# Kernel optimization log

Measured on AMD Instinct MI355X. Metric: run time of the kernel, lower is better.

Reference implementation:

```python
import jax, jax.numpy as jnp
import numpy as np
from jax import lax

# Dimensions (see shape_source)
B, J, I, E, H = 256, 128, 64, 512, 512   # batch, target len, source len, embed, hidden
MAXJW = 128                               # max jump width
WJ = 2 * MAXJW + 1                        # size of jump-width set (257)
ALPHA_P0 = 1.0
EPS = 1e-29


def setup_inputs() -> dict:
    key = jax.random.key(0)
    ks = jax.random.split(key, 10)
    return {
        "y_hidden": jax.random.normal(ks[0], (B, J, E), jnp.float32),
        "y_hidden_null": jax.random.normal(ks[1], (1, 1, E), jnp.float32),
        "W_trans": jax.random.normal(ks[2], (E, H), jnp.float32) * 0.02,
        "b_trans": jnp.zeros((H,), jnp.float32),
        "W_jump": jax.random.normal(ks[3], (H, WJ), jnp.float32) * 0.02,
        "b_jump": jnp.zeros((WJ,), jnp.float32),
        "W_p0": jax.random.normal(ks[4], (H, 1), jnp.float32) * 0.02,
        "b_p0": jnp.zeros((1,), jnp.float32),
        # emission probs p(source_t | target_state_k), kept near 1 to avoid
        # underflow of the unrescaled HMM forward product (as in original).
        "emission": jax.random.uniform(ks[5], (B, 2 * J, I), jnp.float32) * 0.5 + 0.75,
        "source_lengths": jax.random.randint(ks[6], (B,), 1, I + 1, dtype=jnp.int32),
        "target_lengths": jax.random.randint(ks[7], (B,), 1, J + 1, dtype=jnp.int32),
    }


def _build_transition(y_hidden, y_hidden_null, W_trans, b_trans, W_jump, b_jump, W_p0, b_p0):
    # get_transition: Dense(tanh) -> Dense(softmax) jump widths; Dense(sigmoid) p0.
    ts = jnp.tanh(y_hidden @ W_trans + b_trans)           # [B,J,H]
    ts_null = jnp.tanh(y_hidden_null @ W_trans + b_trans) # [1,1,H]
    jump_prob = jax.nn.softmax(ts @ W_jump + b_jump, axis=-1)  # [B,J,WJ]
    p0_scalar = ALPHA_P0 * jax.nn.sigmoid(ts_null @ W_p0 + b_p0)[0, 0, 0]
    p0 = jnp.broadcast_to(p0_scalar, (y_hidden.shape[0], J))  # tile to [B,J]
    # gather jump widths: row i takes jump_prob[:, i, MAXJW + k - i] for k in [0,J)
    idx = MAXJW + jnp.arange(J)[None, :] - jnp.arange(J)[:, None]        # [J,J]
    idxb = jnp.broadcast_to(idx[None], (jump_prob.shape[0], J, J))
    jw = jnp.take_along_axis(jump_prob, idxb, axis=2)                    # [B,J,J]
    jw = jw * (1.0 - p0[:, :, None]) / jnp.sum(jw, axis=2, keepdims=True)
    diag_p0 = p0[:, :, None] * jnp.eye(J, dtype=jw.dtype)                # [B,J,J]
    T_half = jnp.concatenate([jw, diag_p0], axis=2)                      # [B,J,2J]
    return jnp.concatenate([T_half, T_half], axis=1)                     # [B,2J,2J]


def reference(y_hidden, y_hidden_null, W_trans, b_trans, W_jump, b_jump,
              W_p0, b_p0, emission, source_lengths, target_lengths):
    T = _build_transition(y_hidden, y_hidden_null, W_trans, b_trans,
                          W_jump, b_jump, W_p0, b_p0)       # [B,2J,2J]
    e = jnp.transpose(emission, (2, 0, 1))                  # [I,B,2J]
    # tf.scan with no initializer: f_0 = emission at source position 0
    f0 = e[0]

    def step(f, et):
        f_next = jnp.einsum('bj,bjk->bk', f, T) * et        # forward recursion
        return f_next, f_next

    _, fs = lax.scan(step, f0, e[1:])
    fs = jnp.concatenate([f0[None], fs], axis=0)            # [I,B,2J]
    fbt = jnp.transpose(fs, (1, 2, 0))                      # [B,2J,I]
    last_idx = (source_lengths - 1).astype(jnp.int32)[:, None, None]
    last = jnp.take_along_axis(fbt, last_idx, axis=2)[:, :, 0]  # [B,2J]
    m = (jnp.arange(J)[None, :] < target_lengths[:, None]).astype(last.dtype)
    mask = jnp.concatenate([m, m], axis=1)                  # [B,2J]
    return jnp.log(jnp.sum(last * mask, axis=1) + EPS)      # [B]
```

## Files before the change

kernel.cpp:

```cpp
#include <hip/hip_runtime.h>
#include <stdint.h>

typedef __attribute__((ext_vector_type(8))) short bf16x8;
typedef __attribute__((ext_vector_type(4))) float f32x4;

__device__ __forceinline__ unsigned short f2bf(float f) {
  union { float f; unsigned int u; } un; un.f = f;
  unsigned int r = un.u + 0x7fffu + ((un.u >> 16) & 1u);
  return (unsigned short)(r >> 16);
}

__device__ __forceinline__ float tanh_fast(float x) {
  x = fminf(15.f, fmaxf(-15.f, x));
  float e = __expf(2.f * x);
  return (e - 1.f) / (e + 1.f);
}

__device__ __forceinline__ unsigned int cvt_pk_bf16(float lo, float hi) {
  unsigned int r;
  asm("v_cvt_pk_bf16_f32 %0, %1, %2" : "=v"(r) : "v"(lo), "v"(hi));
  return r;
}

__device__ __forceinline__ void gload_lds16(const void* g, void* l) {
  __builtin_amdgcn_global_load_lds(
      (const __attribute__((address_space(1))) unsigned int*)(unsigned long long)g,
      (__attribute__((address_space(3))) unsigned int*)(unsigned int)(unsigned long long)l,
      16, 0, 0);
}

__global__ __launch_bounds__(256) void cvt_transpose_kernel(
    const float* __restrict__ W, unsigned short* __restrict__ Wt,
    int R, int C, int ldW) {
  int i = blockIdx.x * blockDim.x + threadIdx.x;
  if (i < R * C) {
    int c = i / R, r = i - c * R;
    Wt[(size_t)c * R + r] = f2bf(W[(size_t)r * ldW + c]);
  }
}

__global__ __launch_bounds__(512) void p0_kernel(
    const float* __restrict__ ynull, const float* __restrict__ W_trans,
    const float* __restrict__ b_trans, const float* __restrict__ W_p0,
    const float* __restrict__ b_p0, float* __restrict__ p0buf) {
  __shared__ float red[512];
  const int hh = threadIdx.x;
  float acc = 0.f;
  for (int e = 0; e < 512; ++e) acc = fmaf(ynull[e], W_trans[(size_t)e * 512 + hh], acc);
  const float ts = tanhf(acc + b_trans[hh]);
  red[hh] = ts * W_p0[hh];
  __syncthreads();
  for (int s = 256; s > 0; s >>= 1) {
    if (hh < s) red[hh] += red[hh + s];
    __syncthreads();
  }
  if (hh == 0) {
    const float z = red[0] + b_p0[0];
    const float p0 = 1.f / (1.f + __expf(-z));
    p0buf[0] = p0;
    p0buf[1] = 1.f - p0;
  }
}


__global__ __launch_bounds__(256, 2) void gemm_af32(
    const float* __restrict__ A, const unsigned short* __restrict__ Bt,
    const float* __restrict__ bias, unsigned short* __restrict__ Cout,
    int M, int N, int K) {
  __shared__ unsigned short sA[128 * 32];
  __shared__ unsigned short sB[128 * 32];
  const int tid = threadIdx.x;
  const int lane = tid & 63;
  const int wave = tid >> 6;
  const int wr = wave >> 1, wc = wave & 1;
  const int m0 = blockIdx.x * 128, n0 = blockIdx.y * 128;

  f32x4 acc[4][4] = {};

  const int srow = lane >> 2;
  const int sl = lane & 3;
  const int scol = sl * 8;
  const int wsz = (srow >> 1) & 3;
  const int scolw = (sl ^ wsz) * 8;
  const int c0 = wave * 2, c1 = wave * 2 + 1;
  const float* Af0 = A + (size_t)(m0 + c0 * 16 + srow) * K + scol;
  const float* Af1 = A + (size_t)(m0 + c1 * 16 + srow) * K + scol;
  const unsigned short* Br0 = Bt + (size_t)(n0 + c0 * 16 + srow) * K + scolw;
  const unsigned short* Br1 = Bt + (size_t)(n0 + c1 * 16 + srow) * K + scolw;

  float4 a00 = *reinterpret_cast<const float4*>(Af0);
  float4 a01 = *reinterpret_cast<const float4*>(Af0 + 4);
  float4 a10 = *reinterpret_cast<const float4*>(Af1);
  float4 a11 = *reinterpret_cast<const float4*>(Af1 + 4);

  const int r15 = lane & 15;
  const int oslot = (((lane >> 4) ^ ((r15 >> 1) & 3))) * 8;

  for (int kk = 0; kk < K; kk += 32) {
    __syncthreads();
    {
      union { unsigned int u[4]; bf16x8 v; } p;
      p.u[0] = cvt_pk_bf16(a00.x, a00.y);
      p.u[1] = cvt_pk_bf16(a00.z, a00.w);
      p.u[2] = cvt_pk_bf16(a01.x, a01.y);
      p.u[3] = cvt_pk_bf16(a01.z, a01.w);
      *reinterpret_cast<bf16x8*>(&sA[c0 * 512 + srow * 32 + scolw]) = p.v;
      p.u[0] = cvt_pk_bf16(a10.x, a10.y);
      p.u[1] = cvt_pk_bf16(a10.z, a10.w);
      p.u[2] = cvt_pk_bf16(a11.x, a11.y);
      p.u[3] = cvt_pk_bf16(a11.z, a11.w);
      *reinterpret_cast<bf16x8*>(&sA[c1 * 512 + srow * 32 + scolw]) = p.v;
    }
    gload_lds16(Br0 + kk, &sB[c0 * 512]);
    gload_lds16(Br1 + kk, &sB[c1 * 512]);
    __syncthreads();
    if (kk + 32 < K) {
      a00 = *reinterpret_cast<const float4*>(Af0 + kk + 32);
      a01 = *reinterpret_cast<const float4*>(Af0 + kk + 36);
      a10 = *reinterpret_cast<const float4*>(Af1 + kk + 32);
      a11 = *reinterpret_cast<const float4*>(Af1 + kk + 36);
    }
    bf16x8 af[4], bfr[4];
#pragma unroll
    for (int mi = 0; mi < 4; ++mi)
      af[mi] = *reinterpret_cast<const bf16x8*>(
          &sA[(wr * 64 + mi * 16 + r15) * 32 + oslot]);
#pragma unroll
    for (int ni = 0; ni < 4; ++ni)
      bfr[ni] = *reinterpret_cast<const bf16x8*>(
          &sB[(wc * 64 + ni * 16 + r15) * 32 + oslot]);
#pragma unroll
    for (int mi = 0; mi < 4; ++mi)
#pragma unroll
      for (int ni = 0; ni < 4; ++ni)
        acc[mi][ni] = __builtin_amdgcn_mfma_f32_16x16x32_bf16(
            af[mi], bfr[ni], acc[mi][ni], 0, 0, 0);
  }

  const int crow0 = m0 + wr * 64 + (lane >> 4) * 4;
  const int ccol0 = n0 + wc * 64 + r15;
#pragma unroll
  for (int mi = 0; mi < 4; ++mi) {
#pragma unroll
    for (int ni = 0; ni < 4; ++ni) {
      const int gcol = ccol0 + ni * 16;
      const float bv = bias[gcol];
#pragma unroll
      for (int r = 0; r < 4; ++r) {
        const int grow = crow0 + mi * 16 + r;
        Cout[(size_t)grow * N + gcol] = f2bf(tanh_fast(acc[mi][ni][r] + bv));
      }
    }
  }
}

__global__ __launch_bounds__(256, 2) void gemm_tt(
    const unsigned short* __restrict__ A, const unsigned short* __restrict__ Bt,
    const float* __restrict__ bias, float* __restrict__ Cout,
    int M, int N, int K) {
  __shared__ unsigned short sA[128 * 32];
  __shared__ unsigned short sB[128 * 32];
  const int tid = threadIdx.x;
  const int lane = tid & 63;
  const int wave = tid >> 6;
  const int wr = wave >> 1, wc = wave & 1;
  const int m0 = blockIdx.x * 128, n0 = blockIdx.y * 128;

  f32x4 acc[4][4] = {};

  const int srow = lane >> 2;
  const int sl = lane & 3;
  const int wsz = (srow >> 1) & 3;
  const int scolw = (sl ^ wsz) * 8;
  const int c0 = wave * 2, c1 = wave * 2 + 1;
  const unsigned short* Ar0 = A + (size_t)(m0 + c0 * 16 + srow) * K + scolw;
  const unsigned short* Ar1 = A + (size_t)(m0 + c1 * 16 + srow) * K + scolw;
  const unsigned short* Br0 = Bt + (size_t)(n0 + c0 * 16 + srow) * K + scolw;
  const unsigned short* Br1 = Bt + (size_t)(n0 + c1 * 16 + srow) * K + scolw;

  const int r15 = lane & 15;
  const int oslot = (((lane >> 4) ^ ((r15 >> 1) & 3))) * 8;

  for (int kk = 0; kk < K; kk += 32) {
    __syncthreads();
    gload_lds16(Ar0 + kk, &sA[c0 * 512]);
    gload_lds16(Ar1 + kk, &sA[c1 * 512]);
    gload_lds16(Br0 + kk, &sB[c0 * 512]);
    gload_lds16(Br1 + kk, &sB[c1 * 512]);
    __syncthreads();
    bf16x8 af[4], bfr[4];
#pragma unroll
    for (int mi = 0; mi < 4; ++mi)
      af[mi] = *reinterpret_cast<const bf16x8*>(
          &sA[(wr * 64 + mi * 16 + r15) * 32 + oslot]);
#pragma unroll
    for (int ni = 0; ni < 4; ++ni)
      bfr[ni] = *reinterpret_cast<const bf16x8*>(
          &sB[(wc * 64 + ni * 16 + r15) * 32 + oslot]);
#pragma unroll
    for (int mi = 0; mi < 4; ++mi)
#pragma unroll
      for (int ni = 0; ni < 4; ++ni)
        acc[mi][ni] = __builtin_amdgcn_mfma_f32_16x16x32_bf16(
            af[mi], bfr[ni], acc[mi][ni], 0, 0, 0);
  }

  const int crow0 = m0 + wr * 64 + (lane >> 4) * 4;
  const int ccol0 = n0 + wc * 64 + r15;
#pragma unroll
  for (int mi = 0; mi < 4; ++mi) {
#pragma unroll
    for (int ni = 0; ni < 4; ++ni) {
      const int gcol = ccol0 + ni * 16;
      const float bv = bias[gcol];
#pragma unroll
      for (int r = 0; r < 4; ++r) {
        const int grow = crow0 + mi * 16 + r;
        Cout[(size_t)grow * N + gcol] = acc[mi][ni][r] + bv;
      }
    }
  }
}

__global__ __launch_bounds__(256) void wsoftmax_kernel(
    const float* __restrict__ logits, const float* __restrict__ p0buf,
    unsigned short* __restrict__ jwout) {
  const int lane = threadIdx.x & 63;
  const int wave = threadIdx.x >> 6;
  const int row = blockIdx.x * 4 + wave;
  const int i = row & 127;
  const float* lrow = logits + (size_t)row * 256 + (128 - i);
  const float v0 = lrow[lane];
  const float v1 = lrow[lane + 64];
  float mx = fmaxf(v0, v1);
#pragma unroll
  for (int off = 32; off > 0; off >>= 1) mx = fmaxf(mx, __shfl_xor(mx, off));
  const float e0 = __expf(v0 - mx);
  const float e1 = __expf(v1 - mx);
  float s = e0 + e1;
#pragma unroll
  for (int off = 32; off > 0; off >>= 1) s += __shfl_xor(s, off);
  const float scale = p0buf[1] / s;
  unsigned short* orow = jwout + (size_t)row * 128;
  orow[lane] = f2bf(e0 * scale);
  orow[lane + 64] = f2bf(e1 * scale);
}

#define SE_STRIDE 264
__global__ __launch_bounds__(256, 1) void forward_fused(
    const unsigned short* __restrict__ jwb,
    const float* __restrict__ emission,
    const float* __restrict__ p0buf, const int* __restrict__ slen_p,
    const int* __restrict__ tlen_p, float* __restrict__ out) {
  __shared__ __align__(16) float se[64 * SE_STRIDE];
  __shared__ __align__(16) unsigned short gl16[128];
  const int b = blockIdx.x;
  const int tid = threadIdx.x;
  const float* eb = emission + (size_t)b * 16384;

  bf16x8 bfr[4][8];
  const int l = tid & 63;
  const int m = l & 15;
  const int q = l >> 4;

  if (tid >= 64) {
#pragma unroll
    for (int it = 0; it < 6; ++it) {
      const int tau = (tid - 64) + 192 * it;
      if (tau < 1024) {
        const int t0 = (tau & 15) * 4;
        const int mm = (tau >> 4) & 15;
        const int nt0 = ((tau >> 8) & 1) * 4;
        const int half = (tau >> 9) & 1;
        const int kbase = half * 128 + nt0 * 16 + mm;
        const float4 v0 = *reinterpret_cast<const float4*>(&eb[(size_t)(kbase) * 64 + t0]);
        const float4 v1 = *reinterpret_cast<const float4*>(&eb[(size_t)(kbase + 16) * 64 + t0]);
        const float4 v2 = *reinterpret_cast<const float4*>(&eb[(size_t)(kbase + 32) * 64 + t0]);
        const float4 v3 = *reinterpret_cast<const float4*>(&eb[(size_t)(kbase + 48) * 64 + t0]);
        const int jinv0 = half * 128 + mm * 8 + nt0;
        float* d = &se[(size_t)t0 * SE_STRIDE + jinv0];
        *reinterpret_cast<float4*>(d) = (float4){v0.x, v1.x, v2.x, v3.x};
        *reinterpret_cast<float4*>(d + SE_STRIDE) = (float4){v0.y, v1.y, v2.y, v3.y};
        *reinterpret_cast<float4*>(d + 2 * SE_STRIDE) = (float4){v0.z, v1.z, v2.z, v3.z};
        *reinterpret_cast<float4*>(d + 3 * SE_STRIDE) = (float4){v0.w, v1.w, v2.w, v3.w};
      }
    }
  } else {
    const unsigned short* jwt = jwb + (size_t)b * 16384;
#pragma unroll
    for (int kt = 0; kt < 4; ++kt) {
      const int r0 = kt * 32 + q * 8;
#pragma unroll
      for (int nt = 0; nt < 8; ++nt) {
        const int c = nt * 16 + m;
        bf16x8 v;
#pragma unroll
        for (int j = 0; j < 8; ++j) v[j] = (short)jwt[(size_t)(r0 + j) * 128 + c];
        bfr[kt][nt] = v;
      }
    }
  }
  __syncthreads();
  if (tid >= 64) return;

  const float p0 = p0buf[0];
  const int S = slen_p[b];
  const int T = tlen_p[b];

  float gown[8];
  {
    const float4 i0a = *reinterpret_cast<const float4*>(&se[m * 8]);
    const float4 i0b = *reinterpret_cast<const float4*>(&se[m * 8 + 4]);
    const float4 i1a = *reinterpret_cast<const float4*>(&se[128 + m * 8]);
    const float4 i1b = *reinterpret_cast<const float4*>(&se[128 + m * 8 + 4]);
    gown[0] = i0a.x + i1a.x; gown[1] = i0a.y + i1a.y;
    gown[2] = i0a.z + i1a.z; gown[3] = i0a.w + i1a.w;
    gown[4] = i0b.x + i1b.x; gown[5] = i0b.y + i1b.y;
    gown[6] = i0b.z + i1b.z; gown[7] = i0b.w + i1b.w;
  }
  gl16[(2 * q) * 16 + m]     = f2bf(gown[2 * q]);
  gl16[(2 * q + 1) * 16 + m] = f2bf(gown[2 * q + 1]);

  for (int t = 1; t < S; ++t) {
    const float* st = &se[(size_t)t * SE_STRIDE];
    const float4 pe0a = *reinterpret_cast<const float4*>(&st[m * 8]);
    const float4 pe0b = *reinterpret_cast<const float4*>(&st[m * 8 + 4]);
    const float4 pe1a = *reinterpret_cast<const float4*>(&st[128 + m * 8]);
    const float4 pe1b = *reinterpret_cast<const float4*>(&st[128 + m * 8 + 4]);
    const float e0[8] = {pe0a.x, pe0a.y, pe0a.z, pe0a.w, pe0b.x, pe0b.y, pe0b.z, pe0b.w};
    const float e1[8] = {pe1a.x, pe1a.y, pe1a.z, pe1a.w, pe1b.x, pe1b.y, pe1b.z, pe1b.w};
    float h[8];
#pragma unroll
    for (int nt = 0; nt < 8; ++nt) h[nt] = gown[nt] * (p0 * e1[nt]);
    bf16x8 af[4];
#pragma unroll
    for (int kt = 0; kt < 4; ++kt)
      af[kt] = *reinterpret_cast<const bf16x8*>(&gl16[kt * 32 + q * 8]);
    f32x4 acc[8];
#pragma unroll
    for (int nt = 0; nt < 8; ++nt) {
      f32x4 a = __builtin_amdgcn_mfma_f32_16x16x32_bf16(
          af[0], bfr[0][nt], (f32x4){0.f, 0.f, 0.f, 0.f}, 0, 0, 0);
      a = __builtin_amdgcn_mfma_f32_16x16x32_bf16(af[1], bfr[1][nt], a, 0, 0, 0);
      a = __builtin_amdgcn_mfma_f32_16x16x32_bf16(af[2], bfr[2][nt], a, 0, 0, 0);
      acc[nt] = __builtin_amdgcn_mfma_f32_16x16x32_bf16(af[3], bfr[3][nt], a, 0, 0, 0);
    }
#pragma unroll
    for (int nt = 0; nt < 8; ++nt) gown[nt] = fmaf(acc[nt][0], e0[nt], h[nt]);
    gl16[(2 * q) * 16 + m]     = f2bf(gown[2 * q]);
    gl16[(2 * q + 1) * 16 + m] = f2bf(gown[2 * q + 1]);
  }

  float val = 0.f;
#pragma unroll
  for (int nt = 0; nt < 8; ++nt)
    if (nt * 16 + m < T) val += gown[nt];
#pragma unroll
  for (int off = 1; off < 16; off <<= 1) val += __shfl_xor(val, off);
  if (l == 0) out[b] = logf(val + 1e-29f);
}

extern "C" void kernel_launch(void* const* d_in, const int* in_sizes, int n_in,
                              void* d_out, int out_size, void* d_ws, size_t ws_size,
                              hipStream_t stream) {
  const float* y_hidden = (const float*)d_in[0];
  const float* y_null   = (const float*)d_in[1];
  const float* W_trans  = (const float*)d_in[2];
  const float* b_trans  = (const float*)d_in[3];
  const float* W_jump   = (const float*)d_in[4];
  const float* b_jump   = (const float*)d_in[5];
  const float* W_p0     = (const float*)d_in[6];
  const float* b_p0     = (const float*)d_in[7];
  const float* emission = (const float*)d_in[8];
  const int* slen = (const int*)d_in[9];
  const int* tlen = (const int*)d_in[10];
  float* out = (float*)d_out;

  char* ws = (char*)d_ws;
  float* logits         = (float*)ws;
  unsigned short* ts16  = (unsigned short*)(ws + 33554432);
  unsigned short* wt16t = (unsigned short*)(ws + 67108864);
  unsigned short* wj16t = (unsigned short*)(ws + 67633152);
  float* p0buf          = (float*)(ws + 67895296);
  unsigned short* jwb16 = (unsigned short*)(ws + 67895552);

  cvt_transpose_kernel<<<dim3((512 * 512 + 255) / 256), dim3(256), 0, stream>>>(
      W_trans, wt16t, 512, 512, 512);
  cvt_transpose_kernel<<<dim3((512 * 256 + 255) / 256), dim3(256), 0, stream>>>(
      W_jump, wj16t, 512, 256, 257);
  p0_kernel<<<dim3(1), dim3(512), 0, stream>>>(y_null, W_trans, b_trans, W_p0, b_p0, p0buf);

  gemm_af32<<<dim3(256, 4), dim3(256), 0, stream>>>(y_hidden, wt16t, b_trans, ts16,
                                                    32768, 512, 512);
  gemm_tt<<<dim3(256, 2), dim3(256), 0, stream>>>(ts16, wj16t, b_jump, logits,
                                                  32768, 256, 512);
  wsoftmax_kernel<<<dim3(8192), dim3(256), 0, stream>>>(logits, p0buf, jwb16);
  forward_fused<<<dim3(256), dim3(256), 0, stream>>>(jwb16, emission, p0buf,
                                                     slen, tlen, out);
}
```

Measured before the change: 118.6 us.

## Double-buffer GEMM LDS staging, store logits as bf16, merge weight conversion kernels

Result: faster. 116.2 us (-2.0%).

```diff
diff --git a/kernel.cpp b/kernel.cpp
--- a/kernel.cpp
+++ b/kernel.cpp
@@ -8,6 +8,11 @@
   union { float f; unsigned int u; } un; un.f = f;
   unsigned int r = un.u + 0x7fffu + ((un.u >> 16) & 1u);
   return (unsigned short)(r >> 16);
+}
+
+__device__ __forceinline__ float bf2f(unsigned short u) {
+  union { unsigned int u; float f; } un; un.u = ((unsigned int)u) << 16;
+  return un.f;
 }
 
 __device__ __forceinline__ float tanh_fast(float x) {
@@ -29,13 +34,17 @@
       16, 0, 0);
 }
 
-__global__ __launch_bounds__(256) void cvt_transpose_kernel(
-    const float* __restrict__ W, unsigned short* __restrict__ Wt,
-    int R, int C, int ldW) {
-  int i = blockIdx.x * blockDim.x + threadIdx.x;
-  if (i < R * C) {
-    int c = i / R, r = i - c * R;
-    Wt[(size_t)c * R + r] = f2bf(W[(size_t)r * ldW + c]);
+__global__ __launch_bounds__(256) void cvt_weights(
+    const float* __restrict__ Wt_in, const float* __restrict__ Wj_in,
+    unsigned short* __restrict__ wt, unsigned short* __restrict__ wj) {
+  const int i = blockIdx.x * 256 + threadIdx.x;
+  if (i < 512 * 512) {
+    const int c = i >> 9, r = i & 511;
+    wt[i] = f2bf(Wt_in[(size_t)r * 512 + c]);
+  } else {
+    const int j = i - 512 * 512;
+    const int c = j >> 9, r = j & 511;
+    wj[j] = f2bf(Wj_in[(size_t)r * 257 + c]);
   }
 }
 
@@ -67,8 +76,8 @@
     const float* __restrict__ A, const unsigned short* __restrict__ Bt,
     const float* __restrict__ bias, unsigned short* __restrict__ Cout,
     int M, int N, int K) {
-  __shared__ unsigned short sA[128 * 32];
-  __shared__ unsigned short sB[128 * 32];
+  __shared__ unsigned short sA[2][128 * 32];
+  __shared__ unsigned short sB[2][128 * 32];
   const int tid = threadIdx.x;
   const int lane = tid & 63;
   const int wave = tid >> 6;
@@ -88,53 +97,83 @@
   const unsigned short* Br0 = Bt + (size_t)(n0 + c0 * 16 + srow) * K + scolw;
   const unsigned short* Br1 = Bt + (size_t)(n0 + c1 * 16 + srow) * K + scolw;
 
-  float4 a00 = *reinterpret_cast<const float4*>(Af0);
-  float4 a01 = *reinterpret_cast<const float4*>(Af0 + 4);
-  float4 a10 = *reinterpret_cast<const float4*>(Af1);
-  float4 a11 = *reinterpret_cast<const float4*>(Af1 + 4);
-
   const int r15 = lane & 15;
-  const int oslot = (((lane >> 4) ^ ((r15 >> 1) & 3))) * 8;
-
-  for (int kk = 0; kk < K; kk += 32) {
-    __syncthreads();
-    {
-      union { unsigned int u[4]; bf16x8 v; } p;
-      p.u[0] = cvt_pk_bf16(a00.x, a00.y);
-      p.u[1] = cvt_pk_bf16(a00.z, a00.w);
-      p.u[2] = cvt_pk_bf16(a01.x, a01.y);
-      p.u[3] = cvt_pk_bf16(a01.z, a01.w);
-      *reinterpret_cast<bf16x8*>(&sA[c0 * 512 + srow * 32 + scolw]) = p.v;
-      p.u[0] = cvt_pk_bf16(a10.x, a10.y);
-      p.u[1] = cvt_pk_bf16(a10.z, a10.w);
-      p.u[2] = cvt_pk_bf16(a11.x, a11.y);
-      p.u[3] = cvt_pk_bf16(a11.z, a11.w);
-      *reinterpret_cast<bf16x8*>(&sA[c1 * 512 + srow * 32 + scolw]) = p.v;
-    }
-    gload_lds16(Br0 + kk, &sB[c0 * 512]);
-    gload_lds16(Br1 + kk, &sB[c1 * 512]);
-    __syncthreads();
-    if (kk + 32 < K) {
-      a00 = *reinterpret_cast<const float4*>(Af0 + kk + 32);
-      a01 = *reinterpret_cast<const float4*>(Af0 + kk + 36);
-      a10 = *reinterpret_cast<const float4*>(Af1 + kk + 32);
-      a11 = *reinterpret_cast<const float4*>(Af1 + kk + 36);
-    }
+  const int oslot = ((lane >> 4) ^ ((r15 >> 1) & 3)) * 8;
+  const int nt = K >> 5;
+
+  auto writeA = [&](int bi, const float4& v00, const float4& v01,
+                    const float4& v10, const float4& v11) {
+    union { unsigned int u[4]; bf16x8 v; } p;
+    p.u[0] = cvt_pk_bf16(v00.x, v00.y);
+    p.u[1] = cvt_pk_bf16(v00.z, v00.w);
+    p.u[2] = cvt_pk_bf16(v01.x, v01.y);
+    p.u[3] = cvt_pk_bf16(v01.z, v01.w);
+    *reinterpret_cast<bf16x8*>(&sA[bi][c0 * 512 + srow * 32 + scolw]) = p.v;
+    p.u[0] = cvt_pk_bf16(v10.x, v10.y);
+    p.u[1] = cvt_pk_bf16(v10.z, v10.w);
+    p.u[2] = cvt_pk_bf16(v11.x, v11.y);
+    p.u[3] = cvt_pk_bf16(v11.z, v11.w);
+    *reinterpret_cast<bf16x8*>(&sA[bi][c1 * 512 + srow * 32 + scolw]) = p.v;
+  };
+  auto stageB = [&](int bi, int t) {
+    gload_lds16(Br0 + t * 32, &sB[bi][c0 * 512]);
+    gload_lds16(Br1 + t * 32, &sB[bi][c1 * 512]);
+  };
+  auto compute = [&](int bi) {
     bf16x8 af[4], bfr[4];
 #pragma unroll
     for (int mi = 0; mi < 4; ++mi)
       af[mi] = *reinterpret_cast<const bf16x8*>(
-          &sA[(wr * 64 + mi * 16 + r15) * 32 + oslot]);
+          &sA[bi][(wr * 64 + mi * 16 + r15) * 32 + oslot]);
 #pragma unroll
     for (int ni = 0; ni < 4; ++ni)
       bfr[ni] = *reinterpret_cast<const bf16x8*>(
-          &sB[(wc * 64 + ni * 16 + r15) * 32 + oslot]);
+          &sB[bi][(wc * 64 + ni * 16 + r15) * 32 + oslot]);
 #pragma unroll
     for (int mi = 0; mi < 4; ++mi)
 #pragma unroll
       for (int ni = 0; ni < 4; ++ni)
         acc[mi][ni] = __builtin_amdgcn_mfma_f32_16x16x32_bf16(
             af[mi], bfr[ni], acc[mi][ni], 0, 0, 0);
+  };
+
+  float4 x0 = *reinterpret_cast<const float4*>(Af0);
+  float4 x1 = *reinterpret_cast<const float4*>(Af0 + 4);
+  float4 x2 = *reinterpret_cast<const float4*>(Af1);
+  float4 x3 = *reinterpret_cast<const float4*>(Af1 + 4);
+  float4 y0 = *reinterpret_cast<const float4*>(Af0 + 32);
+  float4 y1 = *reinterpret_cast<const float4*>(Af0 + 36);
+  float4 y2 = *reinterpret_cast<const float4*>(Af1 + 32);
+  float4 y3 = *reinterpret_cast<const float4*>(Af1 + 36);
+  writeA(0, x0, x1, x2, x3);
+  stageB(0, 0);
+  __syncthreads();
+
+  for (int t = 0; t < nt; t += 2) {
+    if (t + 1 < nt) {
+      writeA(1, y0, y1, y2, y3);
+      stageB(1, t + 1);
+    }
+    if (t + 2 < nt) {
+      x0 = *reinterpret_cast<const float4*>(Af0 + (t + 2) * 32);
+      x1 = *reinterpret_cast<const float4*>(Af0 + (t + 2) * 32 + 4);
+      x2 = *reinterpret_cast<const float4*>(Af1 + (t + 2) * 32);
+      x3 = *reinterpret_cast<const float4*>(Af1 + (t + 2) * 32 + 4);
+    }
+    compute(0);
+    __syncthreads();
+    if (t + 2 < nt) {
+      writeA(0, x0, x1, x2, x3);
+      stageB(0, t + 2);
+    }
+    if (t + 3 < nt) {
+      y0 = *reinterpret_cast<const float4*>(Af0 + (t + 3) * 32);
+      y1 = *reinterpret_cast<const float4*>(Af0 + (t + 3) * 32 + 4);
+      y2 = *reinterpret_cast<const float4*>(Af1 + (t + 3) * 32);
+      y3 = *reinterpret_cast<const float4*>(Af1 + (t + 3) * 32 + 4);
+    }
+    if (t + 1 < nt) compute(1);
+    __syncthreads();
   }
 
   const int crow0 = m0 + wr * 64 + (lane >> 4) * 4;
@@ -156,10 +195,10 @@
 
 __global__ __launch_bounds__(256, 2) void gemm_tt(
     const unsigned short* __restrict__ A, const unsigned short* __restrict__ Bt,
-    const float* __restrict__ bias, float* __restrict__ Cout,
+    const float* __restrict__ bias, unsigned short* __restrict__ Cout,
     int M, int N, int K) {
-  __shared__ unsigned short sA[128 * 32];
-  __shared__ unsigned short sB[128 * 32];
+  __shared__ unsigned short sA[2][128 * 32];
+  __shared__ unsigned short sB[2][128 * 32];
   const int tid = threadIdx.x;
   const int lane = tid & 63;
   const int wave = tid >> 6;
@@ -179,30 +218,42 @@
   const unsigned short* Br1 = Bt + (size_t)(n0 + c1 * 16 + srow) * K + scolw;
 
   const int r15 = lane & 15;
-  const int oslot = (((lane >> 4) ^ ((r15 >> 1) & 3))) * 8;
-
-  for (int kk = 0; kk < K; kk += 32) {
-    __syncthreads();
-    gload_lds16(Ar0 + kk, &sA[c0 * 512]);
-    gload_lds16(Ar1 + kk, &sA[c1 * 512]);
-    gload_lds16(Br0 + kk, &sB[c0 * 512]);
-    gload_lds16(Br1 + kk, &sB[c1 * 512]);
-    __syncthreads();
+  const int oslot = ((lane >> 4) ^ ((r15 >> 1) & 3)) * 8;
+  const int nt = K >> 5;
+
+  auto stage = [&](int bi, int t) {
+    gload_lds16(Ar0 + t * 32, &sA[bi][c0 * 512]);
+    gload_lds16(Ar1 + t * 32, &sA[bi][c1 * 512]);
+    gload_lds16(Br0 + t * 32, &sB[bi][c0 * 512]);
+    gload_lds16(Br1 + t * 32, &sB[bi][c1 * 512]);
+  };
+  auto compute = [&](int bi) {
     bf16x8 af[4], bfr[4];
 #pragma unroll
     for (int mi = 0; mi < 4; ++mi)
       af[mi] = *reinterpret_cast<const bf16x8*>(
-          &sA[(wr * 64 + mi * 16 + r15) * 32 + oslot]);
+          &sA[bi][(wr * 64 + mi * 16 + r15) * 32 + oslot]);
 #pragma unroll
     for (int ni = 0; ni < 4; ++ni)
       bfr[ni] = *reinterpret_cast<const bf16x8*>(
-          &sB[(wc * 64 + ni * 16 + r15) * 32 + oslot]);
+          &sB[bi][(wc * 64 + ni * 16 + r15) * 32 + oslot]);
 #pragma unroll
     for (int mi = 0; mi < 4; ++mi)
 #pragma unroll
       for (int ni = 0; ni < 4; ++ni)
         acc[mi][ni] = __builtin_amdgcn_mfma_f32_16x16x32_bf16(
             af[mi], bfr[ni], acc[mi][ni], 0, 0, 0);
+  };
+
+  stage(0, 0);
+  __syncthreads();
+  for (int t = 0; t < nt; t += 2) {
+    if (t + 1 < nt) stage(1, t + 1);
+    compute(0);
+    __syncthreads();
+    if (t + 2 < nt) stage(0, t + 2);
+    if (t + 1 < nt) compute(1);
+    __syncthreads();
   }
 
   const int crow0 = m0 + wr * 64 + (lane >> 4) * 4;
@@ -216,22 +267,22 @@
 #pragma unroll
       for (int r = 0; r < 4; ++r) {
         const int grow = crow0 + mi * 16 + r;
-        Cout[(size_t)grow * N + gcol] = acc[mi][ni][r] + bv;
+        Cout[(size_t)grow * N + gcol] = f2bf(acc[mi][ni][r] + bv);
       }
     }
   }
 }
 
 __global__ __launch_bounds__(256) void wsoftmax_kernel(
-    const float* __restrict__ logits, const float* __restrict__ p0buf,
+    const unsigned short* __restrict__ logits, const float* __restrict__ p0buf,
     unsigned short* __restrict__ jwout) {
   const int lane = threadIdx.x & 63;
   const int wave = threadIdx.x >> 6;
   const int row = blockIdx.x * 4 + wave;
   const int i = row & 127;
-  const float* lrow = logits + (size_t)row * 256 + (128 - i);
-  const float v0 = lrow[lane];
-  const float v1 = lrow[lane + 64];
+  const unsigned short* lrow = logits + (size_t)row * 256 + (128 - i);
+  const float v0 = bf2f(lrow[lane]);
+  const float v1 = bf2f(lrow[lane + 64]);
   float mx = fmaxf(v0, v1);
 #pragma unroll
   for (int off = 32; off > 0; off >>= 1) mx = fmaxf(mx, __shfl_xor(mx, off));
@@ -377,24 +428,21 @@
   float* out = (float*)d_out;
 
   char* ws = (char*)d_ws;
-  float* logits         = (float*)ws;
-  unsigned short* ts16  = (unsigned short*)(ws + 33554432);
-  unsigned short* wt16t = (unsigned short*)(ws + 67108864);
-  unsigned short* wj16t = (unsigned short*)(ws + 67633152);
-  float* p0buf          = (float*)(ws + 67895296);
-  unsigned short* jwb16 = (unsigned short*)(ws + 67895552);
-
-  cvt_transpose_kernel<<<dim3((512 * 512 + 255) / 256), dim3(256), 0, stream>>>(
-      W_trans, wt16t, 512, 512, 512);
-  cvt_transpose_kernel<<<dim3((512 * 256 + 255) / 256), dim3(256), 0, stream>>>(
-      W_jump, wj16t, 512, 256, 257);
+  unsigned short* ts16  = (unsigned short*)ws;
+  unsigned short* lg16  = (unsigned short*)(ws + 33554432);
+  unsigned short* wt16t = (unsigned short*)(ws + 50331648);
+  unsigned short* wj16t = (unsigned short*)(ws + 50855936);
+  float* p0buf          = (float*)(ws + 51118080);
+  unsigned short* jwb16 = (unsigned short*)(ws + 51118336);
+
+  cvt_weights<<<dim3(1536), dim3(256), 0, stream>>>(W_trans, W_jump, wt16t, wj16t);
   p0_kernel<<<dim3(1), dim3(512), 0, stream>>>(y_null, W_trans, b_trans, W_p0, b_p0, p0buf);
 
   gemm_af32<<<dim3(256, 4), dim3(256), 0, stream>>>(y_hidden, wt16t, b_trans, ts16,
                                                     32768, 512, 512);
-  gemm_tt<<<dim3(256, 2), dim3(256), 0, stream>>>(ts16, wj16t, b_jump, logits,
+  gemm_tt<<<dim3(256, 2), dim3(256), 0, stream>>>(ts16, wj16t, b_jump, lg16,
                                                   32768, 256, 512);
-  wsoftmax_kernel<<<dim3(8192), dim3(256), 0, stream>>>(logits, p0buf, jwb16);
+  wsoftmax_kernel<<<dim3(8192), dim3(256), 0, stream>>>(lg16, p0buf, jwb16);
   forward_fused<<<dim3(256), dim3(256), 0, stream>>>(jwb16, emission, p0buf,
                                                      slen, tlen, out);
 }
```
